# Optimization experiments

Measured on AMD Instinct MI355X. Metric: run time of the kernel, lower is better.

## Reference

```python
import jax, jax.numpy as jnp
import numpy as np


def setup_inputs() -> dict:
    key = jax.random.key(0)
    k1, k2, k3, k4 = jax.random.split(key, 4)
    B, D_IN, D, N, A = 32, 2048, 128, 400000, 7
    return {
        "x": jax.random.normal(k1, (B, D_IN), dtype=jnp.float32),
        "W_enc": jax.random.normal(k2, (D_IN, D), dtype=jnp.float32) * 0.02,
        "b_enc": jnp.zeros((D,), dtype=jnp.float32),
        "reps": jax.random.normal(k3, (N, D), dtype=jnp.float32),
        "actions": jax.random.normal(k4, (N, A), dtype=jnp.float32),
        "k": 5,
    }


def reference(x, W_enc, b_enc, reps, actions, k):
    # encoder embed: [B, D]
    batch_rep = x @ W_enc + b_enc
    # euclidean cdist: [B, N]
    sq = (
        jnp.sum(batch_rep * batch_rep, axis=-1, keepdims=True)
        + jnp.sum(reps * reps, axis=-1)[None, :]
        - 2.0 * (batch_rep @ reps.T)
    )
    dists = jnp.sqrt(jnp.maximum(sq, 1e-12))
    # top-k smallest distances
    neg_topk, indices = jax.lax.top_k(-dists, k)  # [B, k]
    top_k_distances = -neg_topk
    # gather actions: [B, k, A]
    top_k_actions = actions[indices]
    # softmax(-distance) weights: [B, k]
    weights = jax.nn.softmax(-top_k_distances, axis=1)
    # weighted average: [B, A]
    pred = jnp.sum(top_k_actions * weights[..., None], axis=1)
    return pred
```

## Files before the change

### kernel.cpp

```cpp
#include <hip/hip_runtime.h>
#include <math.h>

#define BATCH 32
#define DIN   2048
#define DK    128
#define NREPS 400000
#define ACT   7
#define TN    128
#define NTILES (NREPS / TN)

__device__ __forceinline__ void topk_insert(float s, int n,
    float& d0, float& d1, float& d2, float& d3, float& d4,
    int& i0, int& i1, int& i2, int& i3, int& i4)
{
    if (s < d4) {
        if (s < d3) {
            d4 = d3; i4 = i3;
            if (s < d2) {
                d3 = d2; i3 = i2;
                if (s < d1) {
                    d2 = d1; i2 = i1;
                    if (s < d0) { d1 = d0; i1 = i0; d0 = s; i0 = n; }
                    else        { d1 = s;  i1 = n; }
                } else { d2 = s; i2 = n; }
            } else { d3 = s; i3 = n; }
        } else { d4 = s; i4 = n; }
    }
}

__global__ __launch_bounds__(256) void encoder_kernel(
    const float* __restrict__ x, const float* __restrict__ W,
    const float* __restrict__ be, float* __restrict__ brept,
    float* __restrict__ brnorm)
{
    __shared__ float xs[DIN];
    __shared__ float part[256];
    __shared__ float vrow[DK];
    const int b = blockIdx.x, t = threadIdx.x;

    const float4* x4 = (const float4*)(x + (size_t)b * DIN);
    float4* xs4 = (float4*)xs;
    xs4[t]       = x4[t];
    xs4[t + 256] = x4[t + 256];
    __syncthreads();

    const int d = t & 127, h = t >> 7;
    const float* Wp = W + (size_t)(h * 1024) * DK + d;
    const float* xp = xs + h * 1024;
    float a0 = 0.f, a1 = 0.f, a2 = 0.f, a3 = 0.f;
    for (int i = 0; i < 1024; i += 4) {
        a0 = fmaf(xp[i],     Wp[(size_t)i * DK],       a0);
        a1 = fmaf(xp[i + 1], Wp[(size_t)(i + 1) * DK], a1);
        a2 = fmaf(xp[i + 2], Wp[(size_t)(i + 2) * DK], a2);
        a3 = fmaf(xp[i + 3], Wp[(size_t)(i + 3) * DK], a3);
    }
    part[t] = (a0 + a1) + (a2 + a3);
    __syncthreads();
    if (t < DK) {
        float v = part[t] + part[t + 128] + be[t];
        brept[t * BATCH + b] = -2.0f * v;
        vrow[t] = v * v;
    }
    __syncthreads();
    if (t == 0) {
        float s = 0.f;
        for (int i = 0; i < DK; i++) s += vrow[i];
        brnorm[b] = s;
    }
}

__global__ __launch_bounds__(256) void dist_topk_kernel(
    const float* __restrict__ reps, const float* __restrict__ brept,
    float* __restrict__ pd, int* __restrict__ pi, int G)
{
    __shared__ float brt[DK * BATCH];
    __shared__ float rpt[TN * DK];

    const int t  = threadIdx.x, g = blockIdx.x;
    const int ng = t & 31, bg = t >> 5;

    {
        const float4* src = (const float4*)brept;
        float4* dst = (float4*)brt;
        #pragma unroll
        for (int i = 0; i < 4; i++) dst[t + 256 * i] = src[t + 256 * i];
    }

    float td0[4], td1[4], td2[4], td3[4], td4[4];
    int   ti0[4], ti1[4], ti2[4], ti3[4], ti4[4];
    #pragma unroll
    for (int i = 0; i < 4; i++) {
        td0[i] = td1[i] = td2[i] = td3[i] = td4[i] = 3.0e38f;
        ti0[i] = ti1[i] = ti2[i] = ti3[i] = ti4[i] = 0;
    }

    const int n_  = t >> 5;
    const int kq_ = t & 31;
    const int swz = (kq_ & 7) << 2;

    for (int tile = g; tile < NTILES; tile += G) {
        const float4* gsrc = (const float4*)(reps + (size_t)tile * (TN * DK));
        float4 v[16];
        #pragma unroll
        for (int i = 0; i < 16; i++) v[i] = gsrc[t + 256 * i];
        __syncthreads();
        #pragma unroll
        for (int i = 0; i < 16; i++) {
            const int n   = n_ + 8 * i;
            const int col = (((n & ~3) ^ swz) | (n & 3));
            const int base = (kq_ * 4) * DK + col;
            rpt[base]          = v[i].x;
            rpt[base + DK]     = v[i].y;
            rpt[base + 2 * DK] = v[i].z;
            rpt[base + 3 * DK] = v[i].w;
        }
        __syncthreads();

        float acc[4][4];
        float nrm[4];
        #pragma unroll
        for (int i = 0; i < 4; i++) {
            nrm[i] = 0.f;
            #pragma unroll
            for (int j = 0; j < 4; j++) acc[i][j] = 0.f;
        }
        const int colb = 4 * ng;
        #pragma unroll 2
        for (int kq = 0; kq < 32; kq++) {
            const int col   = colb ^ ((kq & 7) << 2);
            const int rbase = (kq * 4) * DK + col;
            const int bbase = (kq * 4) * BATCH + 4 * bg;
            #pragma unroll
            for (int j4 = 0; j4 < 4; j4++) {
                const float4 r  = *(const float4*)&rpt[rbase + j4 * DK];
                const float4 bb = *(const float4*)&brt[bbase + j4 * BATCH];
                acc[0][0] = fmaf(bb.x, r.x, acc[0][0]);
                acc[0][1] = fmaf(bb.x, r.y, acc[0][1]);
                acc[0][2] = fmaf(bb.x, r.z, acc[0][2]);
                acc[0][3] = fmaf(bb.x, r.w, acc[0][3]);
                acc[1][0] = fmaf(bb.y, r.x, acc[1][0]);
                acc[1][1] = fmaf(bb.y, r.y, acc[1][1]);
                acc[1][2] = fmaf(bb.y, r.z, acc[1][2]);
                acc[1][3] = fmaf(bb.y, r.w, acc[1][3]);
                acc[2][0] = fmaf(bb.z, r.x, acc[2][0]);
                acc[2][1] = fmaf(bb.z, r.y, acc[2][1]);
                acc[2][2] = fmaf(bb.z, r.z, acc[2][2]);
                acc[2][3] = fmaf(bb.z, r.w, acc[2][3]);
                acc[3][0] = fmaf(bb.w, r.x, acc[3][0]);
                acc[3][1] = fmaf(bb.w, r.y, acc[3][1]);
                acc[3][2] = fmaf(bb.w, r.z, acc[3][2]);
                acc[3][3] = fmaf(bb.w, r.w, acc[3][3]);
                nrm[0] = fmaf(r.x, r.x, nrm[0]);
                nrm[1] = fmaf(r.y, r.y, nrm[1]);
                nrm[2] = fmaf(r.z, r.z, nrm[2]);
                nrm[3] = fmaf(r.w, r.w, nrm[3]);
            }
        }

        const int nbase = tile * TN + 4 * ng;
        #pragma unroll
        for (int i = 0; i < 4; i++) {
            #pragma unroll
            for (int j = 0; j < 4; j++) {
                const float s = acc[i][j] + nrm[j];
                topk_insert(s, nbase + j,
                            td0[i], td1[i], td2[i], td3[i], td4[i],
                            ti0[i], ti1[i], ti2[i], ti3[i], ti4[i]);
            }
        }
    }

    __syncthreads();
    float* candD = rpt;
    int*   candI = (int*)(rpt + 5120);
    float* c2D   = rpt + 10240;
    int*   c2I   = (int*)(rpt + 11520);

    #pragma unroll
    for (int i = 0; i < 4; i++) {
        const int base = ((4 * bg + i) * 32 + ng) * 5;
        candD[base]     = td0[i]; candI[base]     = ti0[i];
        candD[base + 1] = td1[i]; candI[base + 1] = ti1[i];
        candD[base + 2] = td2[i]; candI[base + 2] = ti2[i];
        candD[base + 3] = td3[i]; candI[base + 3] = ti3[i];
        candD[base + 4] = td4[i]; candI[base + 4] = ti4[i];
    }
    __syncthreads();
    {
        const int b = t >> 3, sub = t & 7;
        float d0 = 3.0e38f, d1 = 3.0e38f, d2 = 3.0e38f, d3 = 3.0e38f, d4 = 3.0e38f;
        int   i0 = 0, i1 = 0, i2 = 0, i3 = 0, i4 = 0;
        for (int q = 0; q < 4; q++) {
            const int base = (b * 32 + (sub * 4 + q)) * 5;
            #pragma unroll
            for (int e = 0; e < 5; e++)
                topk_insert(candD[base + e], candI[base + e],
                            d0, d1, d2, d3, d4, i0, i1, i2, i3, i4);
        }
        const int ob = (b * 8 + sub) * 5;
        c2D[ob] = d0; c2D[ob + 1] = d1; c2D[ob + 2] = d2; c2D[ob + 3] = d3; c2D[ob + 4] = d4;
        c2I[ob] = i0; c2I[ob + 1] = i1; c2I[ob + 2] = i2; c2I[ob + 3] = i3; c2I[ob + 4] = i4;
    }
    __syncthreads();
    if (t < 32) {
        const int b = t;
        float d0 = 3.0e38f, d1 = 3.0e38f, d2 = 3.0e38f, d3 = 3.0e38f, d4 = 3.0e38f;
        int   i0 = 0, i1 = 0, i2 = 0, i3 = 0, i4 = 0;
        for (int s2 = 0; s2 < 8; s2++) {
            const int base = (b * 8 + s2) * 5;
            #pragma unroll
            for (int e = 0; e < 5; e++)
                topk_insert(c2D[base + e], c2I[base + e],
                            d0, d1, d2, d3, d4, i0, i1, i2, i3, i4);
        }
        const int ob = (g * BATCH + b) * 5;
        pd[ob] = d0; pd[ob + 1] = d1; pd[ob + 2] = d2; pd[ob + 3] = d3; pd[ob + 4] = d4;
        pi[ob] = i0; pi[ob + 1] = i1; pi[ob + 2] = i2; pi[ob + 3] = i3; pi[ob + 4] = i4;
    }
}

__global__ __launch_bounds__(256) void final_kernel(
    const float* __restrict__ pd, const int* __restrict__ pi,
    const float* __restrict__ brnorm, const float* __restrict__ actions,
    float* __restrict__ out, int G)
{
    __shared__ float lD[256 * 5];
    __shared__ int   lI[256 * 5];
    __shared__ float sD[32 * 5];
    __shared__ int   sI[32 * 5];
    const int b = blockIdx.x, t = threadIdx.x;

    float d0 = 3.0e38f, d1 = 3.0e38f, d2 = 3.0e38f, d3 = 3.0e38f, d4 = 3.0e38f;
    int   i0 = 0, i1 = 0, i2 = 0, i3 = 0, i4 = 0;
    for (int g = t; g < G; g += 256) {
        const int base = (g * BATCH + b) * 5;
        #pragma unroll
        for (int e = 0; e < 5; e++)
            topk_insert(pd[base + e], pi[base + e],
                        d0, d1, d2, d3, d4, i0, i1, i2, i3, i4);
    }
    lD[t * 5] = d0; lD[t * 5 + 1] = d1; lD[t * 5 + 2] = d2; lD[t * 5 + 3] = d3; lD[t * 5 + 4] = d4;
    lI[t * 5] = i0; lI[t * 5 + 1] = i1; lI[t * 5 + 2] = i2; lI[t * 5 + 3] = i3; lI[t * 5 + 4] = i4;
    __syncthreads();
    if (t < 32) {
        d0 = d1 = d2 = d3 = d4 = 3.0e38f; i0 = i1 = i2 = i3 = i4 = 0;
        for (int s = 0; s < 8; s++) {
            const int base = (t * 8 + s) * 5;
            #pragma unroll
            for (int e = 0; e < 5; e++)
                topk_insert(lD[base + e], lI[base + e],
                            d0, d1, d2, d3, d4, i0, i1, i2, i3, i4);
        }
        sD[t * 5] = d0; sD[t * 5 + 1] = d1; sD[t * 5 + 2] = d2; sD[t * 5 + 3] = d3; sD[t * 5 + 4] = d4;
        sI[t * 5] = i0; sI[t * 5 + 1] = i1; sI[t * 5 + 2] = i2; sI[t * 5 + 3] = i3; sI[t * 5 + 4] = i4;
    }
    __syncthreads();
    if (t == 0) {
        d0 = d1 = d2 = d3 = d4 = 3.0e38f; i0 = i1 = i2 = i3 = i4 = 0;
        for (int s = 0; s < 32; s++) {
            const int base = s * 5;
            #pragma unroll
            for (int e = 0; e < 5; e++)
                topk_insert(sD[base + e], sI[base + e],
                            d0, d1, d2, d3, d4, i0, i1, i2, i3, i4);
        }
        const float bn = brnorm[b];
        float dist[5]; int idx[5];
        dist[0] = d0; dist[1] = d1; dist[2] = d2; dist[3] = d3; dist[4] = d4;
        idx[0] = i0; idx[1] = i1; idx[2] = i2; idx[3] = i3; idx[4] = i4;
        float dmin = 3.0e38f;
        #pragma unroll
        for (int e = 0; e < 5; e++) {
            dist[e] = sqrtf(fmaxf(dist[e] + bn, 1e-12f));
            dmin = fminf(dmin, dist[e]);
        }
        float w[5], wsum = 0.f;
        #pragma unroll
        for (int e = 0; e < 5; e++) { w[e] = expf(dmin - dist[e]); wsum += w[e]; }
        const float inv = 1.0f / wsum;
        for (int a = 0; a < ACT; a++) {
            float o = 0.f;
            #pragma unroll
            for (int e = 0; e < 5; e++)
                o = fmaf(w[e], actions[(size_t)idx[e] * ACT + a], o);
            out[b * ACT + a] = o * inv;
        }
    }
}

extern "C" void kernel_launch(void* const* d_in, const int* in_sizes, int n_in,
                              void* d_out, int out_size, void* d_ws, size_t ws_size,
                              hipStream_t stream)
{
    (void)in_sizes; (void)n_in; (void)out_size;
    const float* x       = (const float*)d_in[0];
    const float* W       = (const float*)d_in[1];
    const float* be      = (const float*)d_in[2];
    const float* reps    = (const float*)d_in[3];
    const float* actions = (const float*)d_in[4];

    float* ws     = (float*)d_ws;
    float* brept  = ws;
    float* brnorm = ws + 4096;
    float* pd     = ws + 4224;

    int G = 512;
    {
        const size_t avail_f = ws_size / 4;
        if (avail_f < 4224 + (size_t)G * 320) {
            long fit = ((long)avail_f - 4224) / 320;
            G = (fit < 1) ? 1 : (int)fit;
            if (G > 512) G = 512;
        }
    }
    int* pi = (int*)(pd + (size_t)G * BATCH * 5);

    encoder_kernel  <<<32, 256, 0, stream>>>(x, W, be, brept, brnorm);
    dist_topk_kernel<<<G,  256, 0, stream>>>(reps, brept, pd, pi, G);
    final_kernel    <<<32, 256, 0, stream>>>(pd, pi, brnorm, actions, out_size ? (float*)d_out : (float*)d_out, G);
}
```

Measured before the change: 528.4 us.

## Restructure distance kernel to per-wave row ownership with broadcast batch reads

Rewrites the distance/top-k kernel so each lane of a wave owns one reps row and computes dot products against all 32 batch vectors. Reps rows are read directly from global memory and the batch matrix is read from global memory, with no shared-memory staging of reps tiles and no block barriers inside the main loop. Distances are then transposed through a per-wave shared buffer so each lane maintains a top-5 for one batch element. Grid size rises to 782 blocks with an occupancy hint of 4. The cost is 32 accumulators per lane, uncoalesced strided row loads across lanes, and per-group LDS transposes.

```diff
diff --git a/kernel.cpp b/kernel.cpp
--- a/kernel.cpp
+++ b/kernel.cpp
@@ -6,8 +6,7 @@
 #define DK    128
 #define NREPS 400000
 #define ACT   7
-#define TN    128
-#define NTILES (NREPS / TN)
+#define NGRP  (NREPS / 64)
 
 __device__ __forceinline__ void topk_insert(float s, int n,
     float& d0, float& d1, float& d2, float& d3, float& d4,
@@ -69,153 +68,98 @@
     }
 }
 
-__global__ __launch_bounds__(256) void dist_topk_kernel(
-    const float* __restrict__ reps, const float* __restrict__ brept,
-    float* __restrict__ pd, int* __restrict__ pi, int G)
-{
-    __shared__ float brt[DK * BATCH];
-    __shared__ float rpt[TN * DK];
-
-    const int t  = threadIdx.x, g = blockIdx.x;
-    const int ng = t & 31, bg = t >> 5;
-
+__global__ __launch_bounds__(256, 4) void dist_topk_kernel(
+    const float* __restrict__ reps, const float* __restrict__ brt,
+    float* __restrict__ pd, int* __restrict__ pi, int nwaves)
+{
+    __shared__ float wdist[4 * 64 * 36];
+    const int t = threadIdx.x, g = blockIdx.x;
+    const int wid = t >> 6, ln = t & 63;
+    const int b = ln & 31, h = ln >> 5;
+    float* wd = wdist + wid * (64 * 36);
+
+    float d0 = 3.0e38f, d1 = 3.0e38f, d2 = 3.0e38f, d3 = 3.0e38f, d4 = 3.0e38f;
+    int   i0 = 0, i1 = 0, i2 = 0, i3 = 0, i4 = 0;
+
+    for (int grp = g * 4 + wid; grp < NGRP; grp += nwaves) {
+        const float4* rp = (const float4*)(reps + (size_t)(grp * 64 + ln) * DK);
+        float acc[32];
+        #pragma unroll
+        for (int i = 0; i < 32; i++) acc[i] = 0.f;
+        float nrm = 0.f;
+
+        #pragma unroll 1
+        for (int c = 0; c < 4; c++) {
+            float4 r[8];
+            #pragma unroll
+            for (int q = 0; q < 8; q++) r[q] = rp[c * 8 + q];
+            const float* bp0 = brt + c * 32 * BATCH;
+            #pragma unroll
+            for (int q = 0; q < 8; q++) {
+                const float4 rr = r[q];
+                nrm = fmaf(rr.x, rr.x, nrm);
+                nrm = fmaf(rr.y, rr.y, nrm);
+                nrm = fmaf(rr.z, rr.z, nrm);
+                nrm = fmaf(rr.w, rr.w, nrm);
+                const float* bp = bp0 + q * 4 * BATCH;
+                #pragma unroll
+                for (int bb = 0; bb < 32; bb++) {
+                    float a = acc[bb];
+                    a = fmaf(bp[bb],             rr.x, a);
+                    a = fmaf(bp[BATCH + bb],     rr.y, a);
+                    a = fmaf(bp[2 * BATCH + bb], rr.z, a);
+                    a = fmaf(bp[3 * BATCH + bb], rr.w, a);
+                    acc[bb] = a;
+                }
+            }
+        }
+
+        #pragma unroll
+        for (int q = 0; q < 8; q++) {
+            float4 v;
+            v.x = acc[4 * q]     + nrm;
+            v.y = acc[4 * q + 1] + nrm;
+            v.z = acc[4 * q + 2] + nrm;
+            v.w = acc[4 * q + 3] + nrm;
+            *(float4*)&wd[ln * 36 + 4 * q] = v;
+        }
+        asm volatile("s_waitcnt lgkmcnt(0)" ::: "memory");
+
+        const int nb = grp * 64;
+        #pragma unroll 4
+        for (int s = 0; s < 32; s++) {
+            const int row = h * 32 + s;
+            const float dv = wd[row * 36 + b];
+            topk_insert(dv, nb + row, d0, d1, d2, d3, d4, i0, i1, i2, i3, i4);
+        }
+        asm volatile("s_waitcnt lgkmcnt(0)" ::: "memory");
+    }
+
+    __syncthreads();
+    float* cD = wdist;
+    int*   cI = (int*)(wdist + 1280);
     {
-        const float4* src = (const float4*)brept;
-        float4* dst = (float4*)brt;
-        #pragma unroll
-        for (int i = 0; i < 4; i++) dst[t + 256 * i] = src[t + 256 * i];
-    }
-
-    float td0[4], td1[4], td2[4], td3[4], td4[4];
-    int   ti0[4], ti1[4], ti2[4], ti3[4], ti4[4];
-    #pragma unroll
-    for (int i = 0; i < 4; i++) {
-        td0[i] = td1[i] = td2[i] = td3[i] = td4[i] = 3.0e38f;
-        ti0[i] = ti1[i] = ti2[i] = ti3[i] = ti4[i] = 0;
-    }
-
-    const int n_  = t >> 5;
-    const int kq_ = t & 31;
-    const int swz = (kq_ & 7) << 2;
-
-    for (int tile = g; tile < NTILES; tile += G) {
-        const float4* gsrc = (const float4*)(reps + (size_t)tile * (TN * DK));
-        float4 v[16];
-        #pragma unroll
-        for (int i = 0; i < 16; i++) v[i] = gsrc[t + 256 * i];
-        __syncthreads();
-        #pragma unroll
-        for (int i = 0; i < 16; i++) {
-            const int n   = n_ + 8 * i;
-            const int col = (((n & ~3) ^ swz) | (n & 3));
-            const int base = (kq_ * 4) * DK + col;
-            rpt[base]          = v[i].x;
-            rpt[base + DK]     = v[i].y;
-            rpt[base + 2 * DK] = v[i].z;
-            rpt[base + 3 * DK] = v[i].w;
-        }
-        __syncthreads();
-
-        float acc[4][4];
-        float nrm[4];
-        #pragma unroll
-        for (int i = 0; i < 4; i++) {
-            nrm[i] = 0.f;
-            #pragma unroll
-            for (int j = 0; j < 4; j++) acc[i][j] = 0.f;
-        }
-        const int colb = 4 * ng;
-        #pragma unroll 2
-        for (int kq = 0; kq < 32; kq++) {
-            const int col   = colb ^ ((kq & 7) << 2);
-            const int rbase = (kq * 4) * DK + col;
-            const int bbase = (kq * 4) * BATCH + 4 * bg;
-            #pragma unroll
-            for (int j4 = 0; j4 < 4; j4++) {
-                const float4 r  = *(const float4*)&rpt[rbase + j4 * DK];
-                const float4 bb = *(const float4*)&brt[bbase + j4 * BATCH];
-                acc[0][0] = fmaf(bb.x, r.x, acc[0][0]);
-                acc[0][1] = fmaf(bb.x, r.y, acc[0][1]);
-                acc[0][2] = fmaf(bb.x, r.z, acc[0][2]);
-                acc[0][3] = fmaf(bb.x, r.w, acc[0][3]);
-                acc[1][0] = fmaf(bb.y, r.x, acc[1][0]);
-                acc[1][1] = fmaf(bb.y, r.y, acc[1][1]);
-                acc[1][2] = fmaf(bb.y, r.z, acc[1][2]);
-                acc[1][3] = fmaf(bb.y, r.w, acc[1][3]);
-                acc[2][0] = fmaf(bb.z, r.x, acc[2][0]);
-                acc[2][1] = fmaf(bb.z, r.y, acc[2][1]);
-                acc[2][2] = fmaf(bb.z, r.z, acc[2][2]);
-                acc[2][3] = fmaf(bb.z, r.w, acc[2][3]);
-                acc[3][0] = fmaf(bb.w, r.x, acc[3][0]);
-                acc[3][1] = fmaf(bb.w, r.y, acc[3][1]);
-                acc[3][2] = fmaf(bb.w, r.z, acc[3][2]);
-                acc[3][3] = fmaf(bb.w, r.w, acc[3][3]);
-                nrm[0] = fmaf(r.x, r.x, nrm[0]);
-                nrm[1] = fmaf(r.y, r.y, nrm[1]);
-                nrm[2] = fmaf(r.z, r.z, nrm[2]);
-                nrm[3] = fmaf(r.w, r.w, nrm[3]);
-            }
-        }
-
-        const int nbase = tile * TN + 4 * ng;
-        #pragma unroll
-        for (int i = 0; i < 4; i++) {
-            #pragma unroll
-            for (int j = 0; j < 4; j++) {
-                const float s = acc[i][j] + nrm[j];
-                topk_insert(s, nbase + j,
-                            td0[i], td1[i], td2[i], td3[i], td4[i],
-                            ti0[i], ti1[i], ti2[i], ti3[i], ti4[i]);
-            }
-        }
-    }
-
-    __syncthreads();
-    float* candD = rpt;
-    int*   candI = (int*)(rpt + 5120);
-    float* c2D   = rpt + 10240;
-    int*   c2I   = (int*)(rpt + 11520);
-
-    #pragma unroll
-    for (int i = 0; i < 4; i++) {
-        const int base = ((4 * bg + i) * 32 + ng) * 5;
-        candD[base]     = td0[i]; candI[base]     = ti0[i];
-        candD[base + 1] = td1[i]; candI[base + 1] = ti1[i];
-        candD[base + 2] = td2[i]; candI[base + 2] = ti2[i];
-        candD[base + 3] = td3[i]; candI[base + 3] = ti3[i];
-        candD[base + 4] = td4[i]; candI[base + 4] = ti4[i];
-    }
-    __syncthreads();
-    {
-        const int b = t >> 3, sub = t & 7;
-        float d0 = 3.0e38f, d1 = 3.0e38f, d2 = 3.0e38f, d3 = 3.0e38f, d4 = 3.0e38f;
-        int   i0 = 0, i1 = 0, i2 = 0, i3 = 0, i4 = 0;
-        for (int q = 0; q < 4; q++) {
-            const int base = (b * 32 + (sub * 4 + q)) * 5;
-            #pragma unroll
-            for (int e = 0; e < 5; e++)
-                topk_insert(candD[base + e], candI[base + e],
-                            d0, d1, d2, d3, d4, i0, i1, i2, i3, i4);
-        }
-        const int ob = (b * 8 + sub) * 5;
-        c2D[ob] = d0; c2D[ob + 1] = d1; c2D[ob + 2] = d2; c2D[ob + 3] = d3; c2D[ob + 4] = d4;
-        c2I[ob] = i0; c2I[ob + 1] = i1; c2I[ob + 2] = i2; c2I[ob + 3] = i3; c2I[ob + 4] = i4;
+        const int base = t * 5;
+        cD[base]     = d0; cI[base]     = i0;
+        cD[base + 1] = d1; cI[base + 1] = i1;
+        cD[base + 2] = d2; cI[base + 2] = i2;
+        cD[base + 3] = d3; cI[base + 3] = i3;
+        cD[base + 4] = d4; cI[base + 4] = i4;
     }
     __syncthreads();
     if (t < 32) {
-        const int b = t;
-        float d0 = 3.0e38f, d1 = 3.0e38f, d2 = 3.0e38f, d3 = 3.0e38f, d4 = 3.0e38f;
-        int   i0 = 0, i1 = 0, i2 = 0, i3 = 0, i4 = 0;
-        for (int s2 = 0; s2 < 8; s2++) {
-            const int base = (b * 8 + s2) * 5;
-            #pragma unroll
-            for (int e = 0; e < 5; e++)
-                topk_insert(c2D[base + e], c2I[base + e],
-                            d0, d1, d2, d3, d4, i0, i1, i2, i3, i4);
-        }
-        const int ob = (g * BATCH + b) * 5;
-        pd[ob] = d0; pd[ob + 1] = d1; pd[ob + 2] = d2; pd[ob + 3] = d3; pd[ob + 4] = d4;
-        pi[ob] = i0; pi[ob + 1] = i1; pi[ob + 2] = i2; pi[ob + 3] = i3; pi[ob + 4] = i4;
+        float e0 = 3.0e38f, e1 = 3.0e38f, e2 = 3.0e38f, e3 = 3.0e38f, e4 = 3.0e38f;
+        int   j0 = 0, j1 = 0, j2 = 0, j3 = 0, j4 = 0;
+        for (int j = 0; j < 8; j++) {
+            const int base = (t + 32 * j) * 5;
+            #pragma unroll
+            for (int e = 0; e < 5; e++)
+                topk_insert(cD[base + e], cI[base + e],
+                            e0, e1, e2, e3, e4, j0, j1, j2, j3, j4);
+        }
+        const int ob = (g * BATCH + t) * 5;
+        pd[ob] = e0; pd[ob + 1] = e1; pd[ob + 2] = e2; pd[ob + 3] = e3; pd[ob + 4] = e4;
+        pi[ob] = j0; pi[ob + 1] = j1; pi[ob + 2] = j2; pi[ob + 3] = j3; pi[ob + 4] = j4;
     }
 }
 
@@ -304,18 +248,19 @@
     float* brnorm = ws + 4096;
     float* pd     = ws + 4224;
 
-    int G = 512;
+    int G = 782;
     {
         const size_t avail_f = ws_size / 4;
         if (avail_f < 4224 + (size_t)G * 320) {
             long fit = ((long)avail_f - 4224) / 320;
             G = (fit < 1) ? 1 : (int)fit;
-            if (G > 512) G = 512;
+            if (G > 782) G = 782;
         }
     }
     int* pi = (int*)(pd + (size_t)G * BATCH * 5);
+    const int nwaves = G * 4;
 
     encoder_kernel  <<<32, 256, 0, stream>>>(x, W, be, brept, brnorm);
-    dist_topk_kernel<<<G,  256, 0, stream>>>(reps, brept, pd, pi, G);
-    final_kernel    <<<32, 256, 0, stream>>>(pd, pi, brnorm, actions, out_size ? (float*)d_out : (float*)d_out, G);
-}
+    dist_topk_kernel<<<G,  256, 0, stream>>>(reps, brept, pd, pi, nwaves);
+    final_kernel    <<<32, 256, 0, stream>>>(pd, pi, brnorm, actions, (float*)d_out, G);
+}
```

After: 495.0 us. 6.3% less time.
